# Performance work log

Hardware: AMD Instinct MI355X
Metric: run time of the kernel (lower is better)

## Reference

```python
import jax, jax.numpy as jnp
import numpy as np

N = 100000
H1, D1 = 8, 8          # conv1: 8 heads x 8 dims (concat -> 64)
C = 40                 # num_classes, conv2: 1 head
NEG_SLOPE = 0.2


def gat_layer(x, edge_index, W, a_src, a_dst, b, heads, out_dim, concat):
    # x: [N, F_in], W: [F_in, heads*out_dim], a_*: [heads, out_dim], b: [heads*out_dim] or [out_dim]
    h = (x @ W).reshape(-1, heads, out_dim)                 # [N, H, D]
    s_src = jnp.einsum('nhd,hd->nh', h, a_src)              # [N, H]
    s_dst = jnp.einsum('nhd,hd->nh', h, a_dst)              # [N, H]
    src, dst = edge_index[0], edge_index[1]
    e = jax.nn.leaky_relu(s_src[src] + s_dst[dst], NEG_SLOPE)   # [E, H]
    # segment softmax over incoming edges of each dst node
    m = jax.ops.segment_max(e, dst, num_segments=N)         # [N, H]
    e = jnp.exp(e - m[dst])
    z = jax.ops.segment_sum(e, dst, num_segments=N)         # [N, H]
    alpha = e / (z[dst] + 1e-16)                            # [E, H]
    msg = h[src] * alpha[:, :, None]                        # [E, H, D]
    out = jax.ops.segment_sum(msg, dst, num_segments=N)     # [N, H, D]
    if concat:
        out = out.reshape(-1, heads * out_dim)
    else:
        out = out.mean(axis=1)
    return out + b


def setup_inputs() -> dict:
    key = jax.random.key(0)
    ks = jax.random.split(key, 10)
    F_in = 256
    x = jax.random.normal(ks[0], (N, F_in), dtype=jnp.float32)
    edge_index = jax.random.randint(ks[1], (2, 1600000), 0, N, dtype=jnp.int32)
    sc1 = 1.0 / np.sqrt(F_in)
    W1 = jax.random.normal(ks[2], (F_in, H1 * D1), dtype=jnp.float32) * sc1
    a1_src = jax.random.normal(ks[3], (H1, D1), dtype=jnp.float32) * 0.1
    a1_dst = jax.random.normal(ks[4], (H1, D1), dtype=jnp.float32) * 0.1
    b1 = jnp.zeros((H1 * D1,), dtype=jnp.float32)
    sc2 = 1.0 / np.sqrt(H1 * D1)
    W2 = jax.random.normal(ks[5], (H1 * D1, C), dtype=jnp.float32) * sc2
    a2_src = jax.random.normal(ks[6], (1, C), dtype=jnp.float32) * 0.1
    a2_dst = jax.random.normal(ks[7], (1, C), dtype=jnp.float32) * 0.1
    b2 = jnp.zeros((C,), dtype=jnp.float32)
    return {"x": x, "edge_index": edge_index, "W1": W1, "a1_src": a1_src,
            "a1_dst": a1_dst, "b1": b1, "W2": W2, "a2_src": a2_src,
            "a2_dst": a2_dst, "b2": b2}


def reference(x, edge_index, W1, a1_src, a1_dst, b1, W2, a2_src, a2_dst, b2):
    # eval mode: dropout is identity
    h = gat_layer(x, edge_index, W1, a1_src, a1_dst, b1, H1, D1, concat=True)
    h = jax.nn.elu(h)
    out = gat_layer(h, edge_index, W2, a2_src, a2_dst, b2, 1, C, concat=False)
    return jax.nn.log_softmax(out, axis=1)
```

## Files before the change

kernel.cpp:

```cpp
#include <hip/hip_runtime.h>
#include <math.h>

#define BK 10
#define KNODES 1024
#define MAXNB 128

typedef __attribute__((ext_vector_type(8))) short bf16x8;
typedef __attribute__((ext_vector_type(4))) float f32x4;

__device__ __forceinline__ float bf2f(unsigned short u) {
  return __uint_as_float(((unsigned int)u) << 16);
}
__device__ __forceinline__ unsigned short f2bf(float f) {
  unsigned int i = __float_as_uint(f);
  unsigned int r = i + 0x7FFFu + ((i >> 16) & 1u);
  return (unsigned short)(r >> 16);
}

__global__ __launch_bounds__(256) void prep_kernel(
    const float* __restrict__ W1, const float* __restrict__ W2,
    const float* __restrict__ a2s, const float* __restrict__ a2d,
    unsigned short* __restrict__ whi, unsigned short* __restrict__ wlo,
    float* __restrict__ vas, float* __restrict__ vad,
    unsigned short* __restrict__ h1b, unsigned short* __restrict__ h2b,
    float* __restrict__ s1s, float* __restrict__ s2s,
    int* __restrict__ bpos, int capP, int NN) {
  const int blk = blockIdx.x, t = threadIdx.x;
  if (blk == 0 && t < MAXNB) bpos[t] = t * capP;
  if (blk < 32) {
    if (t < 64) {
      int b = blk, lane = t;
      int kt = b >> 2, ct = b & 3;
      int n = lane & 15, g = lane >> 4;
      unsigned short hb[8], lb[8];
#pragma unroll
      for (int j = 0; j < 8; ++j) {
        int k = kt * 32 + g * 8 + j;
        float wv = W1[k * 64 + ct * 16 + n];
        unsigned short hi = f2bf(wv);
        float rem = wv - bf2f(hi);
        hb[j] = hi;
        lb[j] = f2bf(rem);
      }
      size_t base = ((size_t)b * 64 + lane) * 8;
      *(ushort4*)(whi + base)     = make_ushort4(hb[0], hb[1], hb[2], hb[3]);
      *(ushort4*)(whi + base + 4) = make_ushort4(hb[4], hb[5], hb[6], hb[7]);
      *(ushort4*)(wlo + base)     = make_ushort4(lb[0], lb[1], lb[2], lb[3]);
      *(ushort4*)(wlo + base + 4) = make_ushort4(lb[4], lb[5], lb[6], lb[7]);
    }
  } else if (blk == 32) {
    if (t < 64) {
      float s = 0.f, d = 0.f;
      for (int c = 0; c < 40; ++c) {
        float w = W2[t * 40 + c];
        s += w * a2s[c];
        d += w * a2d[c];
      }
      vas[t] = s;
      vad[t] = d;
    }
  } else if (blk == 33) {
    if (t < 64) {
      h1b[(size_t)NN * 64 + t] = 0;
      if (t < 40) h2b[(size_t)NN * 40 + t] = 0;
      if (t < 8)  s1s[(size_t)NN * 8 + t] = -1e30f;
      if (t == 0) s2s[NN] = -1e30f;
    }
  }
}

__global__ __launch_bounds__(256) void gemm1_mfma_kernel(
    const float* __restrict__ x, const unsigned short* __restrict__ whi,
    const unsigned short* __restrict__ wlo, unsigned short* __restrict__ h1b, int N) {
  const int w = threadIdx.x >> 6, lane = threadIdx.x & 63;
  const int m = lane & 15, g = lane >> 4;
  const int rbase = blockIdx.x * 64 + w * 16;
  int arow = rbase + m;
  if (arow >= N) arow = N - 1;
  const float* xrow = x + (size_t)arow * 256 + g * 8;
  f32x4 acc[4] = {{0.f, 0.f, 0.f, 0.f}, {0.f, 0.f, 0.f, 0.f},
                  {0.f, 0.f, 0.f, 0.f}, {0.f, 0.f, 0.f, 0.f}};
#pragma unroll
  for (int kt = 0; kt < 8; ++kt) {
    float4 a0 = *(const float4*)(xrow + kt * 32);
    float4 a1 = *(const float4*)(xrow + kt * 32 + 4);
    float av[8] = {a0.x, a0.y, a0.z, a0.w, a1.x, a1.y, a1.z, a1.w};
    bf16x8 ahi, alo;
#pragma unroll
    for (int j = 0; j < 8; ++j) {
      unsigned int u = __float_as_uint(av[j]);
      unsigned short hi = (unsigned short)(u >> 16);
      float rem = av[j] - bf2f(hi);
      ahi[j] = (short)hi;
      alo[j] = (short)(__float_as_uint(rem) >> 16);
    }
    const unsigned short* wp = whi + ((size_t)(kt * 4) * 64 + lane) * 8;
    const unsigned short* lp = wlo + ((size_t)(kt * 4) * 64 + lane) * 8;
#pragma unroll
    for (int ct = 0; ct < 4; ++ct) {
      bf16x8 bh = *(const bf16x8*)(wp + (size_t)ct * 64 * 8);
      bf16x8 bl = *(const bf16x8*)(lp + (size_t)ct * 64 * 8);
      acc[ct] = __builtin_amdgcn_mfma_f32_16x16x32_bf16(ahi, bh, acc[ct], 0, 0, 0);
      acc[ct] = __builtin_amdgcn_mfma_f32_16x16x32_bf16(alo, bh, acc[ct], 0, 0, 0);
      acc[ct] = __builtin_amdgcn_mfma_f32_16x16x32_bf16(ahi, bl, acc[ct], 0, 0, 0);
    }
  }
#pragma unroll
  for (int r = 0; r < 4; ++r) {
    int ro = rbase + g * 4 + r;
    if (ro < N) {
#pragma unroll
      for (int ct = 0; ct < 4; ++ct)
        h1b[(size_t)ro * 64 + ct * 16 + m] = f2bf(acc[ct][r]);
    }
  }
}

__global__ void s1_kernel(const unsigned short* __restrict__ h1b,
                          const float* __restrict__ a_src,
                          const float* __restrict__ a_dst, float* __restrict__ s_src,
                          float* __restrict__ s_dst, int N8) {
  int id = blockIdx.x * blockDim.x + threadIdx.x;
  if (id >= N8) return;
  int h = id & 7;
  uint4 raw = *(const uint4*)(h1b + (size_t)id * 8);
  float hv[8];
  hv[0] = bf2f(raw.x & 0xffff); hv[1] = bf2f(raw.x >> 16);
  hv[2] = bf2f(raw.y & 0xffff); hv[3] = bf2f(raw.y >> 16);
  hv[4] = bf2f(raw.z & 0xffff); hv[5] = bf2f(raw.z >> 16);
  hv[6] = bf2f(raw.w & 0xffff); hv[7] = bf2f(raw.w >> 16);
  float ss = 0.f, sd = 0.f;
#pragma unroll
  for (int d = 0; d < 8; ++d) {
    ss = fmaf(hv[d], a_src[h * 8 + d], ss);
    sd = fmaf(hv[d], a_dst[h * 8 + d], sd);
  }
  s_src[id] = ss;
  s_dst[id] = sd;
}

__global__ __launch_bounds__(256) void bin_kernel(const int* __restrict__ src,
                                                  const int* __restrict__ dst,
                                                  int* __restrict__ bpos,
                                                  unsigned int* __restrict__ payload,
                                                  int E, int NB, int capP) {
  __shared__ int hist[MAXNB], soff[MAXNB], base[MAXNB], rnk[MAXNB];
  __shared__ unsigned int stage[4096];
  const int t = threadIdx.x;
  const int e0 = blockIdx.x * 4096;
  if (t < MAXNB) { hist[t] = 0; rnk[t] = 0; }
  __syncthreads();
  for (int j = t; j < 4096; j += 256) {
    int e = e0 + j;
    if (e < E) atomicAdd(&hist[dst[e] >> BK], 1);
  }
  __syncthreads();
  if (t == 0) {
    int acc = 0;
    for (int b = 0; b < NB; ++b) { soff[b] = acc; acc += hist[b]; }
  }
  __syncthreads();
  if (t < NB) {
    int c = hist[t];
    base[t] = c ? atomicAdd(&bpos[t], c) : 0;
  }
  __syncthreads();
  for (int j = t; j < 4096; j += 256) {
    int e = e0 + j;
    if (e < E) {
      int d = dst[e];
      int b = d >> BK;
      int s = src[e];
      int r = atomicAdd(&rnk[b], 1);
      stage[soff[b] + r] = (((unsigned)(d & (KNODES - 1))) << 17) | (unsigned)s;
    }
  }
  __syncthreads();
  int wave = t >> 6, lane = t & 63;
  for (int b = wave; b < NB; b += 4) {
    int len = hist[b], bs = soff[b], gb = base[b];
    int lim = (b + 1) * capP;
    for (int j = lane; j < len; j += 64)
      if (gb + j < lim) payload[gb + j] = stage[bs + j];
  }
}

__global__ __launch_bounds__(1024) void fill2_kernel(const unsigned int* __restrict__ payload,
                                                     const int* __restrict__ bpos,
                                                     int* __restrict__ col,
                                                     int* __restrict__ rbeg,
                                                     int* __restrict__ rend,
                                                     int capP, int NN) {
  __shared__ int cnt[KNODES], scn[KNODES], pos[KNODES];
  const int b = blockIdx.x, t = threadIdx.x;
  cnt[t] = 0;
  __syncthreads();
  const int beg = b * capP;
  int len = bpos[b] - beg;
  if (len > capP) len = capP;
  for (int j = t; j < len; j += 1024) atomicAdd(&cnt[payload[beg + j] >> 17], 1);
  __syncthreads();
  const int myc = cnt[t];
  const int padc = (myc + 7) & ~7;
  scn[t] = padc;
  __syncthreads();
  for (int off = 1; off < 1024; off <<= 1) {
    int v = (t >= off) ? scn[t - off] : 0;
    __syncthreads();
    scn[t] += v;
    __syncthreads();
  }
  const int mystart = b * (capP + 8 * KNODES) + scn[t] - padc;
  const int n = (b << BK) + t;
  if (n < NN) { rbeg[n] = mystart; rend[n] = mystart + padc; }
  pos[t] = mystart;
  __syncthreads();
  for (int j = t; j < len; j += 1024) {
    unsigned int pay = payload[beg + j];
    int p = atomicAdd(&pos[pay >> 17], 1);
    col[p] = (int)(pay & 0x1FFFF);
  }
  __syncthreads();
  for (int j = mystart + myc; j < mystart + padc; ++j) col[j] = NN;
}

__global__ __launch_bounds__(256) void agg1_kernel(
    const int* __restrict__ rbeg, const int* __restrict__ rend,
    const int* __restrict__ col,
    const float* __restrict__ s_src, const float* __restrict__ s_dst,
    const unsigned short* __restrict__ h1b, const float* __restrict__ b1,
    const float* __restrict__ vas, const float* __restrict__ vad,
    unsigned short* __restrict__ helub, float* __restrict__ s2s,
    float* __restrict__ s2d, int N) {
  int wv = threadIdx.x >> 6;
  int l  = threadIdx.x & 63;
  int n  = blockIdx.x * 4 + wv;
  if (n >= N) return;
  const int q  = l >> 3;
  const int hh = l & 7;
  const float sdq = s_dst[n * 8 + hh];
  const int beg = __builtin_amdgcn_readfirstlane(rbeg[n]);
  const int end = __builtin_amdgcn_readfirstlane(rend[n]);
  float z = 0.f, acc = 0.f;
  int e = beg;
  if (((end - beg) >> 3) & 1) {
    int4 ia = *(const int4*)(col + e);
    int4 ib = *(const int4*)(col + e + 4);
    int myidx = col[e + q];
    float pv = s_src[(unsigned)myidx * 8u + (unsigned)hh];
    float tt = pv + sdq;
    tt = fmaxf(tt, 0.2f * tt);
    float w = __expf(tt);
    z += w;
    int idxs[8] = {ia.x, ia.y, ia.z, ia.w, ib.x, ib.y, ib.z, ib.w};
#pragma unroll
    for (int j = 0; j < 8; ++j) {
      float wj = __shfl(w, j * 8 + q, 64);
      unsigned short g = h1b[(unsigned)idxs[j] * 64u + (unsigned)l];
      acc = fmaf(wj, bf2f(g), acc);
    }
    e += 8;
  }
  for (; e < end; e += 16) {
    int4 ia = *(const int4*)(col + e);
    int4 ib = *(const int4*)(col + e + 4);
    int4 ic = *(const int4*)(col + e + 8);
    int4 id = *(const int4*)(col + e + 12);
    int my0 = col[e + q];
    int my1 = col[e + 8 + q];
    float pv0 = s_src[(unsigned)my0 * 8u + (unsigned)hh];
    float pv1 = s_src[(unsigned)my1 * 8u + (unsigned)hh];
    int idxs[16] = {ia.x, ia.y, ia.z, ia.w, ib.x, ib.y, ib.z, ib.w,
                    ic.x, ic.y, ic.z, ic.w, id.x, id.y, id.z, id.w};
    unsigned short gg[16];
#pragma unroll
    for (int j = 0; j < 16; ++j) gg[j] = h1b[(unsigned)idxs[j] * 64u + (unsigned)l];
    float t0 = pv0 + sdq; t0 = fmaxf(t0, 0.2f * t0); float w0 = __expf(t0);
    float t1 = pv1 + sdq; t1 = fmaxf(t1, 0.2f * t1); float w1 = __expf(t1);
    z += w0 + w1;
#pragma unroll
    for (int j = 0; j < 8; ++j) {
      float wj = __shfl(w0, j * 8 + q, 64);
      acc = fmaf(wj, bf2f(gg[j]), acc);
    }
#pragma unroll
    for (int j = 0; j < 8; ++j) {
      float wj = __shfl(w1, j * 8 + q, 64);
      acc = fmaf(wj, bf2f(gg[8 + j]), acc);
    }
  }
  z += __shfl_xor(z, 8); z += __shfl_xor(z, 16); z += __shfl_xor(z, 32);
  float zf = __shfl(z, 9 * q, 64);
  float v = acc / (zf + 1e-16f) + b1[l];
  v = v > 0.f ? v : (__expf(v) - 1.f);
  helub[(size_t)n * 64 + l] = f2bf(v);
  float ps = v * vas[l];
  float pd = v * vad[l];
  for (int off = 32; off > 0; off >>= 1) {
    ps += __shfl_xor(ps, off);
    pd += __shfl_xor(pd, off);
  }
  if (l == 0) { s2s[n] = ps; s2d[n] = pd; }
}

__global__ __launch_bounds__(320) void gemm2_kernel(const unsigned short* __restrict__ heb,
                                                    const float* __restrict__ W2,
                                                    unsigned short* __restrict__ h2b, int N) {
  __shared__ float xs[64][132];
  __shared__ float ws[64][40];
  const int r0 = blockIdx.x * 128;
  const int t  = threadIdx.x;
  const int ty = t / 10;
  const int tx = t % 10;
  for (int idx = t; idx < 1024; idx += 320) {
    int row = idx >> 3;
    int k8  = (idx & 7) << 3;
    uint4 raw = make_uint4(0, 0, 0, 0);
    if (r0 + row < N) raw = *(const uint4*)(heb + (size_t)(r0 + row) * 64 + k8);
    xs[k8 + 0][row] = bf2f(raw.x & 0xffff); xs[k8 + 1][row] = bf2f(raw.x >> 16);
    xs[k8 + 2][row] = bf2f(raw.y & 0xffff); xs[k8 + 3][row] = bf2f(raw.y >> 16);
    xs[k8 + 4][row] = bf2f(raw.z & 0xffff); xs[k8 + 5][row] = bf2f(raw.z >> 16);
    xs[k8 + 6][row] = bf2f(raw.w & 0xffff); xs[k8 + 7][row] = bf2f(raw.w >> 16);
  }
  for (int idx = t; idx < 640; idx += 320) {
    int k  = idx / 10;
    int c4 = (idx % 10) << 2;
    *(float4*)(&ws[k][c4]) = *(const float4*)(W2 + k * 40 + c4);
  }
  __syncthreads();
  float acc[4][4] = {};
#pragma unroll 8
  for (int k = 0; k < 64; ++k) {
    float4 xa = *(const float4*)(&xs[k][ty << 2]);
    float4 wb = *(const float4*)(&ws[k][tx << 2]);
    float xv[4] = {xa.x, xa.y, xa.z, xa.w};
    float wv[4] = {wb.x, wb.y, wb.z, wb.w};
#pragma unroll
    for (int i = 0; i < 4; ++i)
#pragma unroll
      for (int j = 0; j < 4; ++j) acc[i][j] = fmaf(xv[i], wv[j], acc[i][j]);
  }
#pragma unroll
  for (int i = 0; i < 4; ++i) {
    int r = r0 + (ty << 2) + i;
    if (r < N) {
      ushort4 o;
      o.x = f2bf(acc[i][0]); o.y = f2bf(acc[i][1]);
      o.z = f2bf(acc[i][2]); o.w = f2bf(acc[i][3]);
      *(ushort4*)(h2b + (size_t)r * 40 + (tx << 2)) = o;
    }
  }
}

__global__ __launch_bounds__(256) void agg2_kernel(
    const int* __restrict__ rbeg, const int* __restrict__ rend,
    const int* __restrict__ col,
    const float* __restrict__ s2s, const float* __restrict__ s2d,
    const unsigned short* __restrict__ h2b, const float* __restrict__ b2,
    float* __restrict__ out, int N) {
  int wv = threadIdx.x >> 6;
  int l  = threadIdx.x & 63;
  int n  = blockIdx.x * 4 + wv;
  if (n >= N) return;
  const int q = l >> 3;
  const bool act = (l < 40);
  const unsigned lc = act ? (unsigned)l : 0u;
  const float sdv = s2d[n];
  const int beg = __builtin_amdgcn_readfirstlane(rbeg[n]);
  const int end = __builtin_amdgcn_readfirstlane(rend[n]);
  float z = 0.f, acc = 0.f;
  int e = beg;
  if (((end - beg) >> 3) & 1) {
    int4 ia = *(const int4*)(col + e);
    int4 ib = *(const int4*)(col + e + 4);
    int myidx = col[e + q];
    float pv = s2s[myidx];
    float tt = pv + sdv;
    tt = fmaxf(tt, 0.2f * tt);
    float w = __expf(tt);
    z += w;
    int idxs[8] = {ia.x, ia.y, ia.z, ia.w, ib.x, ib.y, ib.z, ib.w};
#pragma unroll
    for (int j = 0; j < 8; ++j) {
      float wj = __shfl(w, j * 8, 64);
      unsigned short g = h2b[(unsigned)idxs[j] * 40u + lc];
      acc = fmaf(wj, bf2f(g), acc);
    }
    e += 8;
  }
  for (; e < end; e += 16) {
    int4 ia = *(const int4*)(col + e);
    int4 ib = *(const int4*)(col + e + 4);
    int4 ic = *(const int4*)(col + e + 8);
    int4 id = *(const int4*)(col + e + 12);
    int my0 = col[e + q];
    int my1 = col[e + 8 + q];
    float pv0 = s2s[my0];
    float pv1 = s2s[my1];
    int idxs[16] = {ia.x, ia.y, ia.z, ia.w, ib.x, ib.y, ib.z, ib.w,
                    ic.x, ic.y, ic.z, ic.w, id.x, id.y, id.z, id.w};
    unsigned short gg[16];
#pragma unroll
    for (int j = 0; j < 16; ++j) gg[j] = h2b[(unsigned)idxs[j] * 40u + lc];
    float t0 = pv0 + sdv; t0 = fmaxf(t0, 0.2f * t0); float w0 = __expf(t0);
    float t1 = pv1 + sdv; t1 = fmaxf(t1, 0.2f * t1); float w1 = __expf(t1);
    z += w0 + w1;
#pragma unroll
    for (int j = 0; j < 8; ++j) {
      float wj = __shfl(w0, j * 8, 64);
      acc = fmaf(wj, bf2f(gg[j]), acc);
    }
#pragma unroll
    for (int j = 0; j < 8; ++j) {
      float wj = __shfl(w1, j * 8, 64);
      acc = fmaf(wj, bf2f(gg[8 + j]), acc);
    }
  }
  z += __shfl_xor(z, 8); z += __shfl_xor(z, 16); z += __shfl_xor(z, 32);
  float v = act ? (acc / (z + 1e-16f) + b2[l]) : -1e30f;
  float m = v;
  for (int off = 32; off > 0; off >>= 1) m = fmaxf(m, __shfl_xor(m, off));
  float ex = act ? __expf(v - m) : 0.f;
  float s = ex;
  for (int off = 32; off > 0; off >>= 1) s += __shfl_xor(s, off);
  if (act) out[(size_t)n * 40 + l] = v - m - logf(s);
}

extern "C" void kernel_launch(void* const* d_in, const int* in_sizes, int n_in,
                              void* d_out, int out_size, void* d_ws, size_t ws_size,
                              hipStream_t stream) {
  const float* x   = (const float*)d_in[0];
  const int*   ei  = (const int*)d_in[1];
  const float* W1  = (const float*)d_in[2];
  const float* a1s = (const float*)d_in[3];
  const float* a1d = (const float*)d_in[4];
  const float* b1  = (const float*)d_in[5];
  const float* W2  = (const float*)d_in[6];
  const float* a2s = (const float*)d_in[7];
  const float* a2d = (const float*)d_in[8];
  const float* b2  = (const float*)d_in[9];
  float* out = (float*)d_out;
  (void)n_in; (void)out_size; (void)ws_size;

  const int NN = in_sizes[0] / 256;
  const int E  = in_sizes[1] / 2;
  const int NB = (NN + KNODES - 1) >> BK;
  const int* esrc = ei;
  const int* edst = ei + E;

  int capP = (E + NB - 1) / NB;
  capP += capP / 4 + capP / 16 + 512;
  capP = (capP + 15) & ~15;

  char* p = (char*)d_ws;
  auto alloc = [&](size_t bytes) -> char* {
    char* q = p;
    p += (bytes + 255) & ~(size_t)255;
    return q;
  };
  unsigned short* h1b   = (unsigned short*)alloc((size_t)(NN + 1) * 64 * 2);
  unsigned short* helub = (unsigned short*)alloc((size_t)NN * 64 * 2);
  unsigned short* h2b   = (unsigned short*)alloc((size_t)(NN + 1) * 40 * 2);
  float* s1s  = (float*)alloc((size_t)(NN + 1) * 8 * 4);
  float* s1d  = (float*)alloc((size_t)NN * 8 * 4);
  float* s2s  = (float*)alloc((size_t)(NN + 1) * 4);
  float* s2d  = (float*)alloc((size_t)NN * 4);
  int*   rbeg = (int*)alloc((size_t)NN * 4);
  int*   rend = (int*)alloc((size_t)NN * 4);
  int*   bpos = (int*)alloc(MAXNB * 4);
  unsigned int* payload = (unsigned int*)alloc((size_t)NB * capP * 4);
  int*   col  = (int*)alloc((size_t)NB * (capP + 8 * KNODES) * 4);
  float* vas  = (float*)alloc(64 * 4);
  float* vad  = (float*)alloc(64 * 4);
  unsigned short* w1hi = (unsigned short*)alloc(32 * 64 * 8 * 2);
  unsigned short* w1lo = (unsigned short*)alloc(32 * 64 * 8 * 2);

  prep_kernel<<<34, 256, 0, stream>>>(W1, W2, a2s, a2d, w1hi, w1lo, vas, vad,
                                      h1b, h2b, s1s, s2s, bpos, capP, NN);
  bin_kernel<<<(E + 4095) / 4096, 256, 0, stream>>>(esrc, edst, bpos, payload, E, NB, capP);
  fill2_kernel<<<NB, 1024, 0, stream>>>(payload, bpos, col, rbeg, rend, capP, NN);
  gemm1_mfma_kernel<<<(NN + 63) / 64, 256, 0, stream>>>(x, w1hi, w1lo, h1b, NN);
  s1_kernel<<<(NN * 8 + 255) / 256, 256, 0, stream>>>(h1b, a1s, a1d, s1s, s1d, NN * 8);
  agg1_kernel<<<(NN + 3) / 4, 256, 0, stream>>>(rbeg, rend, col, s1s, s1d, h1b, b1,
                                                vas, vad, helub, s2s, s2d, NN);
  gemm2_kernel<<<(NN + 127) / 128, 320, 0, stream>>>(helub, W2, h2b, NN);
  agg2_kernel<<<(NN + 3) / 4, 256, 0, stream>>>(rbeg, rend, col, s2s, s2d, h2b, b2, out, NN);
}
```

Before: 363.8 us.

## Fuse attention scores into GEMM1 and layer-2 projection into agg1

The layer-1 attention score computation moves into the MFMA GEMM epilogue, using fp32 accumulators and lane shuffles, so the separate s1 kernel is no longer needed. The second-layer linear projection (64x40 with W2) is fused into agg1: each block stages W2 in shared memory, keeps the ELU outputs in shared memory, and writes h2 directly. This removes the helub intermediate buffer round trip and two kernel launches. In exchange, agg1 gains 10KB of shared memory, a block barrier and extra per-block W2 loads, which may reduce occupancy of this latency-bound gather kernel. Scores are now computed from fp32 values rather than bf16-rounded h1.

```diff
diff --git a/kernel.cpp b/kernel.cpp
--- a/kernel.cpp
+++ b/kernel.cpp
@@ -71,7 +71,9 @@
 
 __global__ __launch_bounds__(256) void gemm1_mfma_kernel(
     const float* __restrict__ x, const unsigned short* __restrict__ whi,
-    const unsigned short* __restrict__ wlo, unsigned short* __restrict__ h1b, int N) {
+    const unsigned short* __restrict__ wlo, const float* __restrict__ a1s,
+    const float* __restrict__ a1d, unsigned short* __restrict__ h1b,
+    float* __restrict__ s_src, float* __restrict__ s_dst, int N) {
   const int w = threadIdx.x >> 6, lane = threadIdx.x & 63;
   const int m = lane & 15, g = lane >> 4;
   const int rbase = blockIdx.x * 64 + w * 16;
@@ -114,29 +116,31 @@
         h1b[(size_t)ro * 64 + ct * 16 + m] = f2bf(acc[ct][r]);
     }
   }
-}
-
-__global__ void s1_kernel(const unsigned short* __restrict__ h1b,
-                          const float* __restrict__ a_src,
-                          const float* __restrict__ a_dst, float* __restrict__ s_src,
-                          float* __restrict__ s_dst, int N8) {
-  int id = blockIdx.x * blockDim.x + threadIdx.x;
-  if (id >= N8) return;
-  int h = id & 7;
-  uint4 raw = *(const uint4*)(h1b + (size_t)id * 8);
-  float hv[8];
-  hv[0] = bf2f(raw.x & 0xffff); hv[1] = bf2f(raw.x >> 16);
-  hv[2] = bf2f(raw.y & 0xffff); hv[3] = bf2f(raw.y >> 16);
-  hv[4] = bf2f(raw.z & 0xffff); hv[5] = bf2f(raw.z >> 16);
-  hv[6] = bf2f(raw.w & 0xffff); hv[7] = bf2f(raw.w >> 16);
-  float ss = 0.f, sd = 0.f;
-#pragma unroll
-  for (int d = 0; d < 8; ++d) {
-    ss = fmaf(hv[d], a_src[h * 8 + d], ss);
-    sd = fmaf(hv[d], a_dst[h * 8 + d], sd);
-  }
-  s_src[id] = ss;
-  s_dst[id] = sd;
+  float as_c[4], ad_c[4];
+#pragma unroll
+  for (int ct = 0; ct < 4; ++ct) {
+    int hh = ct * 2 + (m >> 3);
+    int dd = m & 7;
+    as_c[ct] = a1s[hh * 8 + dd];
+    ad_c[ct] = a1d[hh * 8 + dd];
+  }
+#pragma unroll
+  for (int r = 0; r < 4; ++r) {
+    int ro = rbase + g * 4 + r;
+#pragma unroll
+    for (int ct = 0; ct < 4; ++ct) {
+      float ps = acc[ct][r] * as_c[ct];
+      float pd = acc[ct][r] * ad_c[ct];
+      ps += __shfl_xor(ps, 1); pd += __shfl_xor(pd, 1);
+      ps += __shfl_xor(ps, 2); pd += __shfl_xor(pd, 2);
+      ps += __shfl_xor(ps, 4); pd += __shfl_xor(pd, 4);
+      if ((m & 7) == 0 && ro < N) {
+        int hh = ct * 2 + (m >> 3);
+        s_src[ro * 8 + hh] = ps;
+        s_dst[ro * 8 + hh] = pd;
+      }
+    }
+  }
 }
 
 __global__ __launch_bounds__(256) void bin_kernel(const int* __restrict__ src,
@@ -230,124 +234,99 @@
     const float* __restrict__ s_src, const float* __restrict__ s_dst,
     const unsigned short* __restrict__ h1b, const float* __restrict__ b1,
     const float* __restrict__ vas, const float* __restrict__ vad,
-    unsigned short* __restrict__ helub, float* __restrict__ s2s,
-    float* __restrict__ s2d, int N) {
-  int wv = threadIdx.x >> 6;
-  int l  = threadIdx.x & 63;
-  int n  = blockIdx.x * 4 + wv;
-  if (n >= N) return;
-  const int q  = l >> 3;
-  const int hh = l & 7;
-  const float sdq = s_dst[n * 8 + hh];
-  const int beg = __builtin_amdgcn_readfirstlane(rbeg[n]);
-  const int end = __builtin_amdgcn_readfirstlane(rend[n]);
-  float z = 0.f, acc = 0.f;
-  int e = beg;
-  if (((end - beg) >> 3) & 1) {
-    int4 ia = *(const int4*)(col + e);
-    int4 ib = *(const int4*)(col + e + 4);
-    int myidx = col[e + q];
-    float pv = s_src[(unsigned)myidx * 8u + (unsigned)hh];
-    float tt = pv + sdq;
-    tt = fmaxf(tt, 0.2f * tt);
-    float w = __expf(tt);
-    z += w;
-    int idxs[8] = {ia.x, ia.y, ia.z, ia.w, ib.x, ib.y, ib.z, ib.w};
-#pragma unroll
-    for (int j = 0; j < 8; ++j) {
-      float wj = __shfl(w, j * 8 + q, 64);
-      unsigned short g = h1b[(unsigned)idxs[j] * 64u + (unsigned)l];
-      acc = fmaf(wj, bf2f(g), acc);
-    }
-    e += 8;
-  }
-  for (; e < end; e += 16) {
-    int4 ia = *(const int4*)(col + e);
-    int4 ib = *(const int4*)(col + e + 4);
-    int4 ic = *(const int4*)(col + e + 8);
-    int4 id = *(const int4*)(col + e + 12);
-    int my0 = col[e + q];
-    int my1 = col[e + 8 + q];
-    float pv0 = s_src[(unsigned)my0 * 8u + (unsigned)hh];
-    float pv1 = s_src[(unsigned)my1 * 8u + (unsigned)hh];
-    int idxs[16] = {ia.x, ia.y, ia.z, ia.w, ib.x, ib.y, ib.z, ib.w,
-                    ic.x, ic.y, ic.z, ic.w, id.x, id.y, id.z, id.w};
-    unsigned short gg[16];
-#pragma unroll
-    for (int j = 0; j < 16; ++j) gg[j] = h1b[(unsigned)idxs[j] * 64u + (unsigned)l];
-    float t0 = pv0 + sdq; t0 = fmaxf(t0, 0.2f * t0); float w0 = __expf(t0);
-    float t1 = pv1 + sdq; t1 = fmaxf(t1, 0.2f * t1); float w1 = __expf(t1);
-    z += w0 + w1;
-#pragma unroll
-    for (int j = 0; j < 8; ++j) {
-      float wj = __shfl(w0, j * 8 + q, 64);
-      acc = fmaf(wj, bf2f(gg[j]), acc);
-    }
-#pragma unroll
-    for (int j = 0; j < 8; ++j) {
-      float wj = __shfl(w1, j * 8 + q, 64);
-      acc = fmaf(wj, bf2f(gg[8 + j]), acc);
-    }
-  }
-  z += __shfl_xor(z, 8); z += __shfl_xor(z, 16); z += __shfl_xor(z, 32);
-  float zf = __shfl(z, 9 * q, 64);
-  float v = acc / (zf + 1e-16f) + b1[l];
-  v = v > 0.f ? v : (__expf(v) - 1.f);
-  helub[(size_t)n * 64 + l] = f2bf(v);
-  float ps = v * vas[l];
-  float pd = v * vad[l];
-  for (int off = 32; off > 0; off >>= 1) {
-    ps += __shfl_xor(ps, off);
-    pd += __shfl_xor(pd, off);
-  }
-  if (l == 0) { s2s[n] = ps; s2d[n] = pd; }
-}
-
-__global__ __launch_bounds__(320) void gemm2_kernel(const unsigned short* __restrict__ heb,
-                                                    const float* __restrict__ W2,
-                                                    unsigned short* __restrict__ h2b, int N) {
-  __shared__ float xs[64][132];
-  __shared__ float ws[64][40];
-  const int r0 = blockIdx.x * 128;
+    const float* __restrict__ W2, unsigned short* __restrict__ h2b,
+    float* __restrict__ s2s, float* __restrict__ s2d, int N) {
+  __shared__ float W2s[2560];
+  __shared__ float vbuf[4][64];
   const int t  = threadIdx.x;
-  const int ty = t / 10;
-  const int tx = t % 10;
-  for (int idx = t; idx < 1024; idx += 320) {
-    int row = idx >> 3;
-    int k8  = (idx & 7) << 3;
-    uint4 raw = make_uint4(0, 0, 0, 0);
-    if (r0 + row < N) raw = *(const uint4*)(heb + (size_t)(r0 + row) * 64 + k8);
-    xs[k8 + 0][row] = bf2f(raw.x & 0xffff); xs[k8 + 1][row] = bf2f(raw.x >> 16);
-    xs[k8 + 2][row] = bf2f(raw.y & 0xffff); xs[k8 + 3][row] = bf2f(raw.y >> 16);
-    xs[k8 + 4][row] = bf2f(raw.z & 0xffff); xs[k8 + 5][row] = bf2f(raw.z >> 16);
-    xs[k8 + 6][row] = bf2f(raw.w & 0xffff); xs[k8 + 7][row] = bf2f(raw.w >> 16);
-  }
-  for (int idx = t; idx < 640; idx += 320) {
-    int k  = idx / 10;
-    int c4 = (idx % 10) << 2;
-    *(float4*)(&ws[k][c4]) = *(const float4*)(W2 + k * 40 + c4);
-  }
-  __syncthreads();
-  float acc[4][4] = {};
-#pragma unroll 8
-  for (int k = 0; k < 64; ++k) {
-    float4 xa = *(const float4*)(&xs[k][ty << 2]);
-    float4 wb = *(const float4*)(&ws[k][tx << 2]);
-    float xv[4] = {xa.x, xa.y, xa.z, xa.w};
-    float wv[4] = {wb.x, wb.y, wb.z, wb.w};
-#pragma unroll
-    for (int i = 0; i < 4; ++i)
-#pragma unroll
-      for (int j = 0; j < 4; ++j) acc[i][j] = fmaf(xv[i], wv[j], acc[i][j]);
-  }
-#pragma unroll
-  for (int i = 0; i < 4; ++i) {
-    int r = r0 + (ty << 2) + i;
-    if (r < N) {
-      ushort4 o;
-      o.x = f2bf(acc[i][0]); o.y = f2bf(acc[i][1]);
-      o.z = f2bf(acc[i][2]); o.w = f2bf(acc[i][3]);
-      *(ushort4*)(h2b + (size_t)r * 40 + (tx << 2)) = o;
+  const int wv = t >> 6;
+  const int l  = t & 63;
+  const int n  = blockIdx.x * 4 + wv;
+  for (int i = t; i < 2560; i += 256) W2s[i] = W2[i];
+  const bool active = (n < N);
+  float v = 0.f;
+  if (active) {
+    const int q  = l >> 3;
+    const int hh = l & 7;
+    const float sdq = s_dst[n * 8 + hh];
+    const int beg = __builtin_amdgcn_readfirstlane(rbeg[n]);
+    const int end = __builtin_amdgcn_readfirstlane(rend[n]);
+    float z = 0.f, acc = 0.f;
+    int e = beg;
+    if (((end - beg) >> 3) & 1) {
+      int4 ia = *(const int4*)(col + e);
+      int4 ib = *(const int4*)(col + e + 4);
+      int myidx = col[e + q];
+      float pv = s_src[(unsigned)myidx * 8u + (unsigned)hh];
+      float tt = pv + sdq;
+      tt = fmaxf(tt, 0.2f * tt);
+      float w = __expf(tt);
+      z += w;
+      int idxs[8] = {ia.x, ia.y, ia.z, ia.w, ib.x, ib.y, ib.z, ib.w};
+#pragma unroll
+      for (int j = 0; j < 8; ++j) {
+        float wj = __shfl(w, j * 8 + q, 64);
+        unsigned short g = h1b[(unsigned)idxs[j] * 64u + (unsigned)l];
+        acc = fmaf(wj, bf2f(g), acc);
+      }
+      e += 8;
+    }
+    for (; e < end; e += 16) {
+      int4 ia = *(const int4*)(col + e);
+      int4 ib = *(const int4*)(col + e + 4);
+      int4 ic = *(const int4*)(col + e + 8);
+      int4 id = *(const int4*)(col + e + 12);
+      int my0 = col[e + q];
+      int my1 = col[e + 8 + q];
+      float pv0 = s_src[(unsigned)my0 * 8u + (unsigned)hh];
+      float pv1 = s_src[(unsigned)my1 * 8u + (unsigned)hh];
+      int idxs[16] = {ia.x, ia.y, ia.z, ia.w, ib.x, ib.y, ib.z, ib.w,
+                      ic.x, ic.y, ic.z, ic.w, id.x, id.y, id.z, id.w};
+      unsigned short gg[16];
+#pragma unroll
+      for (int j = 0; j < 16; ++j) gg[j] = h1b[(unsigned)idxs[j] * 64u + (unsigned)l];
+      float t0 = pv0 + sdq; t0 = fmaxf(t0, 0.2f * t0); float w0 = __expf(t0);
+      float t1 = pv1 + sdq; t1 = fmaxf(t1, 0.2f * t1); float w1 = __expf(t1);
+      z += w0 + w1;
+#pragma unroll
+      for (int j = 0; j < 8; ++j) {
+        float wj = __shfl(w0, j * 8 + q, 64);
+        acc = fmaf(wj, bf2f(gg[j]), acc);
+      }
+#pragma unroll
+      for (int j = 0; j < 8; ++j) {
+        float wj = __shfl(w1, j * 8 + q, 64);
+        acc = fmaf(wj, bf2f(gg[8 + j]), acc);
+      }
+    }
+    z += __shfl_xor(z, 8); z += __shfl_xor(z, 16); z += __shfl_xor(z, 32);
+    float zf = __shfl(z, 9 * q, 64);
+    v = acc / (zf + 1e-16f) + b1[l];
+    v = v > 0.f ? v : (__expf(v) - 1.f);
+    float ps = v * vas[l];
+    float pd = v * vad[l];
+    for (int off = 32; off > 0; off >>= 1) {
+      ps += __shfl_xor(ps, off);
+      pd += __shfl_xor(pd, off);
+    }
+    if (l == 0) { s2s[n] = ps; s2d[n] = pd; }
+  }
+  vbuf[wv][l] = v;
+  __syncthreads();
+  if (t < 160) {
+    int row = t / 40, c = t % 40;
+    int nn = blockIdx.x * 4 + row;
+    if (nn < N) {
+      float a2 = 0.f;
+#pragma unroll
+      for (int k = 0; k < 64; k += 4) {
+        float4 vv = *(const float4*)&vbuf[row][k];
+        a2 = fmaf(vv.x, W2s[(k + 0) * 40 + c], a2);
+        a2 = fmaf(vv.y, W2s[(k + 1) * 40 + c], a2);
+        a2 = fmaf(vv.z, W2s[(k + 2) * 40 + c], a2);
+        a2 = fmaf(vv.w, W2s[(k + 3) * 40 + c], a2);
+      }
+      h2b[(size_t)nn * 40 + c] = f2bf(a2);
     }
   }
 }
@@ -459,7 +438,6 @@
     return q;
   };
   unsigned short* h1b   = (unsigned short*)alloc((size_t)(NN + 1) * 64 * 2);
-  unsigned short* helub = (unsigned short*)alloc((size_t)NN * 64 * 2);
   unsigned short* h2b   = (unsigned short*)alloc((size_t)(NN + 1) * 40 * 2);
   float* s1s  = (float*)alloc((size_t)(NN + 1) * 8 * 4);
   float* s1d  = (float*)alloc((size_t)NN * 8 * 4);
@@ -479,10 +457,9 @@
                                       h1b, h2b, s1s, s2s, bpos, capP, NN);
   bin_kernel<<<(E + 4095) / 4096, 256, 0, stream>>>(esrc, edst, bpos, payload, E, NB, capP);
   fill2_kernel<<<NB, 1024, 0, stream>>>(payload, bpos, col, rbeg, rend, capP, NN);
-  gemm1_mfma_kernel<<<(NN + 63) / 64, 256, 0, stream>>>(x, w1hi, w1lo, h1b, NN);
-  s1_kernel<<<(NN * 8 + 255) / 256, 256, 0, stream>>>(h1b, a1s, a1d, s1s, s1d, NN * 8);
+  gemm1_mfma_kernel<<<(NN + 63) / 64, 256, 0, stream>>>(x, w1hi, w1lo, a1s, a1d,
+                                                        h1b, s1s, s1d, NN);
   agg1_kernel<<<(NN + 3) / 4, 256, 0, stream>>>(rbeg, rend, col, s1s, s1d, h1b, b1,
-                                                vas, vad, helub, s2s, s2d, NN);
-  gemm2_kernel<<<(NN + 127) / 128, 320, 0, stream>>>(helub, W2, h2b, NN);
+                                                vas, vad, W2, h2b, s2s, s2d, NN);
   agg2_kernel<<<(NN + 3) / 4, 256, 0, stream>>>(rbeg, rend, col, s2s, s2d, h2b, b2, out, NN);
 }
```

Measured after the change: 397.9 us. 1.09x slower.
